# Performance work log

Measured on AMD Instinct MI355X. Metric: run time of the kernel, lower is better.

Reference implementation:

```python
import jax, jax.numpy as jnp
import numpy as np

BOS_IDX = 1
B, T, E, H, V = 32, 128, 512, 1024, 32000


def setup_inputs() -> dict:
    key = jax.random.key(0)
    ks = jax.random.split(key, 8)
    s = 0.02  # small init scale to keep gates in active range
    return {
        "encoder_outputs": jax.random.normal(ks[0], (B, T, H), jnp.float32),
        "encoder_hidden": jax.random.normal(ks[1], (1, B, H), jnp.float32),
        "target_tensor": jax.random.randint(ks[2], (B, T), 0, V),
        "embedding": jax.random.normal(ks[3], (V, E), jnp.float32) * s,
        "W_ih": jax.random.normal(ks[4], (3 * H, E), jnp.float32) * s,
        "W_hh": jax.random.normal(ks[5], (3 * H, H), jnp.float32) * s,
        "b_ih": jnp.zeros((3 * H,), jnp.float32),
        "b_hh": jnp.zeros((3 * H,), jnp.float32),
        "W_out": jax.random.normal(ks[6], (V, H), jnp.float32) * s,
        "b_out": jnp.zeros((V,), jnp.float32),
    }


def _gru_cell(x, h, W_ih, W_hh, b_ih, b_hh):
    # PyTorch GRUCell math, gate order (r, z, n)
    gi = x @ W_ih.T + b_ih          # [B, 3H]
    gh = h @ W_hh.T + b_hh          # [B, 3H]
    i_r, i_z, i_n = jnp.split(gi, 3, axis=-1)
    h_r, h_z, h_n = jnp.split(gh, 3, axis=-1)
    r = jax.nn.sigmoid(i_r + h_r)
    z = jax.nn.sigmoid(i_z + h_z)
    n = jnp.tanh(i_n + r * h_n)
    return (1.0 - z) * n + z * h


def reference(encoder_outputs, encoder_hidden, target_tensor, embedding,
              W_ih, W_hh, b_ih, b_hh, W_out, b_out):
    Bv, Tv = target_tensor.shape
    # teacher forcing: inputs are [BOS, target[:, 0], ..., target[:, T-2]]
    bos = jnp.full((Bv, 1), BOS_IDX, dtype=target_tensor.dtype)
    tokens = jnp.concatenate([bos, target_tensor[:, :-1]], axis=1)  # [B, T]
    h0 = encoder_hidden[0]  # num_layers == 1 -> [B, H]

    def step(h, tok):
        x = jax.nn.relu(embedding[tok])                    # [B, E]
        h_new = _gru_cell(x, h, W_ih, W_hh, b_ih, b_hh)    # [B, H]
        logits = h_new @ W_out.T + b_out                   # [B, V]
        return h_new, logits

    h_final, logits = jax.lax.scan(step, h0, tokens.T)     # logits: [T, B, V]
    log_probs = jax.nn.log_softmax(jnp.transpose(logits, (1, 0, 2)), axis=-1)
    return log_probs, h_final[None]  # decoder_hidden = [1, B, H]
```

## Files before the change

kernel.cpp:

```cpp
#include <hip/hip_runtime.h>

using u16 = unsigned short;
using u32 = unsigned int;
using u64 = unsigned long long;
typedef __attribute__((ext_vector_type(8))) short bf16x8;
typedef __attribute__((ext_vector_type(4))) float f32x4;

#define B_ 32
#define T_ 128
#define E_ 512
#define H_ 1024
#define V_ 32000
#define NROW 4096
#define BTV ((size_t)B_ * T_ * V_)
#define NREC 32
#define NWK 224
#define GRID_MEGA (NREC + NWK)
#define NTN 250
#define NTILES (32 * NTN)
#define NT_STRIDE 256

#define AGENT __HIP_MEMORY_SCOPE_AGENT
#define RLX __ATOMIC_RELAXED

__device__ __forceinline__ u16 f2bf(float f) {
  u32 x = __float_as_uint(f);
  x += 0x7FFFu + ((x >> 16) & 1u);
  return (u16)(x >> 16);
}

__device__ __forceinline__ void gload_lds16(const void* g, void* l) {
  __builtin_amdgcn_global_load_lds(
      (const __attribute__((address_space(1))) u32*)g,
      (__attribute__((address_space(3))) u32*)l, 16, 0, 0);
}

__device__ __forceinline__ float sigm(float x) { return 1.f / (1.f + __expf(-x)); }

__global__ void cast_bf16_kernel(const float* __restrict__ src, u16* __restrict__ dst, int n4) {
  int i = blockIdx.x * blockDim.x + threadIdx.x;
  int stride = gridDim.x * blockDim.x;
  for (; i < n4; i += stride) {
    float4 v = reinterpret_cast<const float4*>(src)[i];
    u32 p0 = (u32)f2bf(v.x) | ((u32)f2bf(v.y) << 16);
    u32 p1 = (u32)f2bf(v.z) | ((u32)f2bf(v.w) << 16);
    reinterpret_cast<uint2*>(dst)[i] = make_uint2(p0, p1);
  }
}

__global__ void embed_kernel(const int* __restrict__ tgt, const float* __restrict__ emb,
                             u16* __restrict__ X) {
  int r = blockIdx.x * 2 + (threadIdx.x >> 7);
  int c = threadIdx.x & 127;
  int t = r & 127;
  int tok = (t == 0) ? 1 : tgt[r - 1];
  float4 v = reinterpret_cast<const float4*>(emb + (size_t)tok * E_)[c];
  u32 p0 = (u32)f2bf(fmaxf(v.x, 0.f)) | ((u32)f2bf(fmaxf(v.y, 0.f)) << 16);
  u32 p1 = (u32)f2bf(fmaxf(v.z, 0.f)) | ((u32)f2bf(fmaxf(v.w, 0.f)) << 16);
  reinterpret_cast<uint2*>(X + (size_t)r * E_)[c] = make_uint2(p0, p1);
}

__global__ __launch_bounds__(256)
void gemm_bt_kernel(const u16* __restrict__ A, const u16* __restrict__ B,
                    const float* __restrict__ bias, float* __restrict__ C,
                    int K, int N) {
  __shared__ __align__(16) u16 As[128 * 32];
  __shared__ __align__(16) u16 Bs[128 * 32];
  int bid = blockIdx.x;
  int mtile = bid & 31, ntile = bid >> 5;
  int m0 = mtile << 7, n0 = ntile << 7;
  int tid = threadIdx.x, wv = tid >> 6, ln = tid & 63;
  int lr = ln & 15, lg = ln >> 4;
  int wrow = (wv >> 1) << 6, wcol = (wv & 1) << 6;

  f32x4 acc[4][4];
#pragma unroll
  for (int m = 0; m < 4; ++m)
#pragma unroll
    for (int n = 0; n < 4; ++n) acc[m][n] = (f32x4){0.f, 0.f, 0.f, 0.f};

  int c0 = tid, c1 = tid + 256;
  const u16* gA0 = A + (size_t)(m0 + (c0 >> 2)) * K + ((c0 & 3) << 3);
  const u16* gA1 = A + (size_t)(m0 + (c1 >> 2)) * K + ((c1 & 3) << 3);
  const u16* gB0 = B + (size_t)(n0 + (c0 >> 2)) * K + ((c0 & 3) << 3);
  const u16* gB1 = B + (size_t)(n0 + (c1 >> 2)) * K + ((c1 & 3) << 3);
  u16* lA0 = As + (wv << 9);
  u16* lA1 = As + 2048 + (wv << 9);
  u16* lB0 = Bs + (wv << 9);
  u16* lB1 = Bs + 2048 + (wv << 9);

  for (int k0 = 0; k0 < K; k0 += 32) {
    gload_lds16(gA0 + k0, lA0);
    gload_lds16(gA1 + k0, lA1);
    gload_lds16(gB0 + k0, lB0);
    gload_lds16(gB1 + k0, lB1);
    __syncthreads();
    bf16x8 a[4], b[4];
#pragma unroll
    for (int m = 0; m < 4; ++m)
      a[m] = *reinterpret_cast<const bf16x8*>(&As[(wrow + (m << 4) + lr) * 32 + (lg << 3)]);
#pragma unroll
    for (int n = 0; n < 4; ++n)
      b[n] = *reinterpret_cast<const bf16x8*>(&Bs[(wcol + (n << 4) + lr) * 32 + (lg << 3)]);
#pragma unroll
    for (int m = 0; m < 4; ++m)
#pragma unroll
      for (int n = 0; n < 4; ++n)
        acc[m][n] = __builtin_amdgcn_mfma_f32_16x16x32_bf16(a[m], b[n], acc[m][n], 0, 0, 0);
    __syncthreads();
  }

#pragma unroll
  for (int m = 0; m < 4; ++m) {
    int rowb = m0 + wrow + (m << 4) + (lg << 2);
#pragma unroll
    for (int n = 0; n < 4; ++n) {
      int col = n0 + wcol + (n << 4) + lr;
      float bvn = bias[col];
#pragma unroll
      for (int i = 0; i < 4; ++i)
        C[(size_t)(rowb + i) * N + col] = acc[m][n][i] + bvn;
    }
  }
}

__global__ __launch_bounds__(256)
void mega_kernel(const u16* __restrict__ Whh16, const float* __restrict__ Gi,
                 const float* __restrict__ bhh, const float* __restrict__ enc_h,
                 u16* __restrict__ hb16, u16* __restrict__ Hall,
                 const u16* __restrict__ Wout16,
                 const float* __restrict__ bout, float* __restrict__ out,
                 float* __restrict__ pM, float* __restrict__ pS,
                 float* __restrict__ outTail, u32* __restrict__ flags) {
  __shared__ __align__(16) char smem[49152];
  int bid = blockIdx.x, tid = threadIdx.x;
  int wv = tid >> 6, ln = tid & 63, lr = ln & 15, lg = ln >> 4;

  if (bid < NREC) {
    int j0 = bid << 5;
    int kb = wv << 8;
    float (*red)[2][6][256] = (float(*)[2][6][256])smem;

    bf16x8 wf[6][8];
#pragma unroll
    for (int g = 0; g < 3; ++g)
#pragma unroll
      for (int nh = 0; nh < 2; ++nh) {
        const u16* wrow = Whh16 + (size_t)(g * H_ + j0 + nh * 16 + lr) * H_ + kb + (lg << 3);
#pragma unroll
        for (int kk = 0; kk < 8; ++kk)
          wf[g * 2 + nh][kk] = *reinterpret_cast<const bf16x8*>(wrow + kk * 32);
      }

    int bb = tid >> 3;
    int j4 = (tid & 7) << 2;
    float4 bhr = *reinterpret_cast<const float4*>(bhh + 0 * H_ + j0 + j4);
    float4 bhz = *reinterpret_cast<const float4*>(bhh + 1 * H_ + j0 + j4);
    float4 bhn = *reinterpret_cast<const float4*>(bhh + 2 * H_ + j0 + j4);
    float4 hp = *reinterpret_cast<const float4*>(enc_h + bb * H_ + j0 + j4);

    for (int t = 0; t < T_; ++t) {
      int cur = t & 1, nxt = cur ^ 1;

      const float* gib = Gi + (size_t)(bb * T_ + t) * (3 * H_) + j0 + j4;
      float4 gir = *reinterpret_cast<const float4*>(gib + 0 * H_);
      float4 giz = *reinterpret_cast<const float4*>(gib + 1 * H_);
      float4 gin = *reinterpret_cast<const float4*>(gib + 2 * H_);

      if (t > 0) {
        if (ln < 8) {
          while (__hip_atomic_load(&flags[(wv * 8 + ln) * 16], RLX, AGENT) < (u32)t)
            __builtin_amdgcn_s_sleep(1);
        }
      }

      const u16* hbase = hb16 + (size_t)cur * (B_ * H_) + kb + (lg << 3);
      f32x4 acc[2][6];
#pragma unroll
      for (int mt = 0; mt < 2; ++mt)
#pragma unroll
        for (int tn = 0; tn < 6; ++tn) acc[mt][tn] = (f32x4){0.f, 0.f, 0.f, 0.f};
#pragma unroll
      for (int kk = 0; kk < 8; ++kk) {
        const u64* p0 = reinterpret_cast<const u64*>(hbase + (size_t)lr * H_ + kk * 32);
        const u64* p1 = reinterpret_cast<const u64*>(hbase + (size_t)(16 + lr) * H_ + kk * 32);
        union { u64 q[2]; bf16x8 v; } A0, A1;
        A0.q[0] = __hip_atomic_load(p0, RLX, AGENT);
        A0.q[1] = __hip_atomic_load(p0 + 1, RLX, AGENT);
        A1.q[0] = __hip_atomic_load(p1, RLX, AGENT);
        A1.q[1] = __hip_atomic_load(p1 + 1, RLX, AGENT);
#pragma unroll
        for (int tn = 0; tn < 6; ++tn) {
          acc[0][tn] = __builtin_amdgcn_mfma_f32_16x16x32_bf16(A0.v, wf[tn][kk], acc[0][tn], 0, 0, 0);
          acc[1][tn] = __builtin_amdgcn_mfma_f32_16x16x32_bf16(A1.v, wf[tn][kk], acc[1][tn], 0, 0, 0);
        }
      }

#pragma unroll
      for (int mt = 0; mt < 2; ++mt)
#pragma unroll
        for (int tn = 0; tn < 6; ++tn)
#pragma unroll
          for (int i = 0; i < 4; ++i)
            red[wv][mt][tn][((lg << 2) + i) * 16 + lr] = acc[mt][tn][i];
      __syncthreads();

      int mt = bb >> 4;
      int nh = j4 >> 4;
      int rbase = (bb & 15) * 16 + (j4 & 15);
      float4 s[3];
#pragma unroll
      for (int g = 0; g < 3; ++g) {
        float4 a4 = make_float4(0.f, 0.f, 0.f, 0.f);
#pragma unroll
        for (int w = 0; w < 4; ++w) {
          float4 v = *reinterpret_cast<const float4*>(&red[w][mt][g * 2 + nh][rbase]);
          a4.x += v.x; a4.y += v.y; a4.z += v.z; a4.w += v.w;
        }
        s[g] = a4;
      }

      float hn[4];
      {
        float r0 = sigm(gir.x + s[0].x + bhr.x);
        float r1 = sigm(gir.y + s[0].y + bhr.y);
        float r2 = sigm(gir.z + s[0].z + bhr.z);
        float r3 = sigm(gir.w + s[0].w + bhr.w);
        float z0 = sigm(giz.x + s[1].x + bhz.x);
        float z1 = sigm(giz.y + s[1].y + bhz.y);
        float z2 = sigm(giz.z + s[1].z + bhz.z);
        float z3 = sigm(giz.w + s[1].w + bhz.w);
        float a0 = gin.x + r0 * (s[2].x + bhn.x);
        float a1 = gin.y + r1 * (s[2].y + bhn.y);
        float a2 = gin.z + r2 * (s[2].z + bhn.z);
        float a3 = gin.w + r3 * (s[2].w + bhn.w);
        float n0 = 2.f / (1.f + __expf(-2.f * a0)) - 1.f;
        float n1 = 2.f / (1.f + __expf(-2.f * a1)) - 1.f;
        float n2 = 2.f / (1.f + __expf(-2.f * a2)) - 1.f;
        float n3 = 2.f / (1.f + __expf(-2.f * a3)) - 1.f;
        hn[0] = (1.f - z0) * n0 + z0 * hp.x;
        hn[1] = (1.f - z1) * n1 + z1 * hp.y;
        hn[2] = (1.f - z2) * n2 + z2 * hp.z;
        hn[3] = (1.f - z3) * n3 + z3 * hp.w;
        hp = make_float4(hn[0], hn[1], hn[2], hn[3]);
      }

      u32 p0 = (u32)f2bf(hn[0]) | ((u32)f2bf(hn[1]) << 16);
      u32 p1 = (u32)f2bf(hn[2]) | ((u32)f2bf(hn[3]) << 16);
      u64 pv = (u64)p0 | ((u64)p1 << 32);

      __hip_atomic_store(reinterpret_cast<u64*>(Hall + (size_t)(t * B_ + bb) * H_ + j0 + j4),
                         pv, RLX, AGENT);
      if (t < T_ - 1) {
        __hip_atomic_store(reinterpret_cast<u64*>(hb16 + (size_t)nxt * (B_ * H_) + bb * H_ + j0 + j4),
                           pv, RLX, AGENT);
      } else {
        reinterpret_cast<float4*>(outTail + (size_t)bb * H_ + j0 + j4)[0] = hp;
      }
      __syncthreads();
      if (tid == 0)
        __hip_atomic_store(&flags[bid * 16], (u32)(t + 1), RLX, AGENT);
    }
    return;
  }

  int wid = bid - NREC;
  u16* As = (u16*)smem;
  u16* Bs = (u16*)(smem + 8192);
  float* pmh = (float*)(smem + 16384);
  float* psh = (float*)(smem + 17408);
  int wrow = (wv >> 1) << 6, wcol = (wv & 1) << 6;

  for (int tau = wid; tau < NTILES; tau += NWK) {
    int m = tau / NTN, n = tau - m * NTN;
    int target = 4 * (m + 1);
    if (tid < NREC) {
      while ((int)__hip_atomic_load(&flags[tid * 16], RLX, AGENT) < target)
        __builtin_amdgcn_s_sleep(32);
    }
    __syncthreads();

    int m0 = m << 7, n0 = n << 7;
    f32x4 acc[4][4];
#pragma unroll
    for (int mi = 0; mi < 4; ++mi)
#pragma unroll
      for (int ni = 0; ni < 4; ++ni) acc[mi][ni] = (f32x4){0.f, 0.f, 0.f, 0.f};

    int c0 = tid, c1 = tid + 256;
    const u16* gA0 = Hall + (size_t)(m0 + (c0 >> 2)) * H_ + ((c0 & 3) << 3);
    const u16* gA1 = Hall + (size_t)(m0 + (c1 >> 2)) * H_ + ((c1 & 3) << 3);
    const u16* gB0 = Wout16 + (size_t)(n0 + (c0 >> 2)) * H_ + ((c0 & 3) << 3);
    const u16* gB1 = Wout16 + (size_t)(n0 + (c1 >> 2)) * H_ + ((c1 & 3) << 3);
    u16* lA0 = As + (wv << 9);
    u16* lA1 = As + 2048 + (wv << 9);
    u16* lB0 = Bs + (wv << 9);
    u16* lB1 = Bs + 2048 + (wv << 9);

    for (int k0 = 0; k0 < H_; k0 += 32) {
      gload_lds16(gA0 + k0, lA0);
      gload_lds16(gA1 + k0, lA1);
      gload_lds16(gB0 + k0, lB0);
      gload_lds16(gB1 + k0, lB1);
      __syncthreads();
      bf16x8 a[4], b[4];
#pragma unroll
      for (int mi = 0; mi < 4; ++mi)
        a[mi] = *reinterpret_cast<const bf16x8*>(&As[(wrow + (mi << 4) + lr) * 32 + (lg << 3)]);
#pragma unroll
      for (int ni = 0; ni < 4; ++ni)
        b[ni] = *reinterpret_cast<const bf16x8*>(&Bs[(wcol + (ni << 4) + lr) * 32 + (lg << 3)]);
#pragma unroll
      for (int mi = 0; mi < 4; ++mi)
#pragma unroll
        for (int ni = 0; ni < 4; ++ni)
          acc[mi][ni] = __builtin_amdgcn_mfma_f32_16x16x32_bf16(a[mi], b[ni], acc[mi][ni], 0, 0, 0);
      __syncthreads();
    }

    float bv[4];
#pragma unroll
    for (int ni = 0; ni < 4; ++ni) bv[ni] = bout[n0 + wcol + (ni << 4) + lr];

#pragma unroll
    for (int mi = 0; mi < 4; ++mi) {
#pragma unroll
      for (int i = 0; i < 4; ++i) {
        int row = wrow + (mi << 4) + (lg << 2) + i;
        int r = m0 + row;
        int rg = (r & 31) * T_ + (r >> 5);
        float* crow = out + (size_t)rg * V_;
        float v[4];
#pragma unroll
        for (int ni = 0; ni < 4; ++ni) {
          v[ni] = acc[mi][ni][i] + bv[ni];
          crow[n0 + wcol + (ni << 4) + lr] = v[ni];
        }
        float vm = fmaxf(fmaxf(v[0], v[1]), fmaxf(v[2], v[3]));
        vm = fmaxf(vm, __shfl_xor(vm, 1));
        vm = fmaxf(vm, __shfl_xor(vm, 2));
        vm = fmaxf(vm, __shfl_xor(vm, 4));
        vm = fmaxf(vm, __shfl_xor(vm, 8));
        float se = __expf(v[0] - vm) + __expf(v[1] - vm) +
                   __expf(v[2] - vm) + __expf(v[3] - vm);
        se += __shfl_xor(se, 1);
        se += __shfl_xor(se, 2);
        se += __shfl_xor(se, 4);
        se += __shfl_xor(se, 8);
        if (lr == 0) { pmh[(wv & 1) * 128 + row] = vm; psh[(wv & 1) * 128 + row] = se; }
      }
    }
    __syncthreads();
    if (tid < 128) {
      float m0v = pmh[tid], m1v = pmh[128 + tid];
      float M = fmaxf(m0v, m1v);
      float S = psh[tid] * __expf(m0v - M) + psh[128 + tid] * __expf(m1v - M);
      int r = m0 + tid;
      int rg = (r & 31) * T_ + (r >> 5);
      pM[(size_t)rg * NT_STRIDE + n] = M;
      pS[(size_t)rg * NT_STRIDE + n] = S;
    }
    __syncthreads();
  }
}

__global__ __launch_bounds__(512)
void lse_fused_kernel(const float* __restrict__ pM, const float* __restrict__ pS,
                      float* __restrict__ out) {
  int r = blockIdx.x;
  int tid = threadIdx.x, wv = tid >> 6, ln = tid & 63;
  float M = -3.0e38f, S = 0.f;
  if (tid < NTN) { M = pM[(size_t)r * NT_STRIDE + tid]; S = pS[(size_t)r * NT_STRIDE + tid]; }
#pragma unroll
  for (int o = 32; o; o >>= 1) {
    float Mo = __shfl_xor(M, o);
    float So = __shfl_xor(S, o);
    float Mn = fmaxf(M, Mo);
    S = S * __expf(M - Mn) + So * __expf(Mo - Mn);
    M = Mn;
  }
  __shared__ float tM[8], tS[8], lsh;
  if (ln == 0) { tM[wv] = M; tS[wv] = S; }
  __syncthreads();
  if (tid == 0) {
    float Mf = tM[0], Sf = tS[0];
    for (int w = 1; w < 8; ++w) {
      float Mn = fmaxf(Mf, tM[w]);
      Sf = Sf * __expf(Mf - Mn) + tS[w] * __expf(tM[w] - Mn);
      Mf = Mn;
    }
    lsh = Mf + __logf(Sf);
  }
  __syncthreads();
  float l = lsh;
  float4* p = reinterpret_cast<float4*>(out + (size_t)r * V_);
  for (int i = tid; i < V_ / 4; i += 512) {
    float4 v = p[i];
    v.x -= l; v.y -= l; v.z -= l; v.w -= l;
    p[i] = v;
  }
}

extern "C" void kernel_launch(void* const* d_in, const int* in_sizes, int n_in,
                              void* d_out, int out_size, void* d_ws, size_t ws_size,
                              hipStream_t stream) {
  const float* enc_h = (const float*)d_in[1];
  const int*   tgt   = (const int*)d_in[2];
  const float* emb   = (const float*)d_in[3];
  const float* Wih   = (const float*)d_in[4];
  const float* Whh   = (const float*)d_in[5];
  const float* bih   = (const float*)d_in[6];
  const float* bhh   = (const float*)d_in[7];
  const float* Wout  = (const float*)d_in[8];
  const float* bout  = (const float*)d_in[9];
  float* out = (float*)d_out;

  char* ws = (char*)d_ws;
  size_t off = 0;
  auto alloc = [&](size_t bytes) -> void* {
    void* p = ws + off;
    off = (off + bytes + 255) & ~(size_t)255;
    return p;
  };
  u32*  flags  = (u32*)alloc(4096);
  u16*  Wih16  = (u16*)alloc((size_t)3 * H_ * E_ * 2);
  u16*  Whh16  = (u16*)alloc((size_t)3 * H_ * H_ * 2);
  u16*  Wout16 = (u16*)alloc((size_t)V_ * H_ * 2);
  u16*  X16    = (u16*)alloc((size_t)NROW * E_ * 2);
  u16*  Hall   = (u16*)alloc((size_t)NROW * H_ * 2);
  u16*  hb16   = (u16*)alloc((size_t)2 * B_ * H_ * 2);
  float* Gi    = (float*)alloc((size_t)NROW * 3 * H_ * 4);
  float* pM    = (float*)alloc((size_t)NROW * NT_STRIDE * 4);
  float* pS    = (float*)alloc((size_t)NROW * NT_STRIDE * 4);

  hipMemsetAsync(flags, 0, 4096, stream);
  cast_bf16_kernel<<<1024, 256, 0, stream>>>(Wih, Wih16, 3 * H_ * E_ / 4);
  cast_bf16_kernel<<<1024, 256, 0, stream>>>(Whh, Whh16, 3 * H_ * H_ / 4);
  cast_bf16_kernel<<<2048, 256, 0, stream>>>(Wout, Wout16, V_ * H_ / 4);
  cast_bf16_kernel<<<32, 256, 0, stream>>>(enc_h, hb16, B_ * H_ / 4);
  embed_kernel<<<NROW / 2, 256, 0, stream>>>(tgt, emb, X16);

  gemm_bt_kernel<<<(3 * H_ / 128) * 32, 256, 0, stream>>>(X16, Wih16, bih, Gi, E_, 3 * H_);

  mega_kernel<<<GRID_MEGA, 256, 0, stream>>>(Whh16, Gi, bhh, enc_h, hb16, Hall,
                                             Wout16, bout, out, pM, pS,
                                             out + BTV, flags);

  lse_fused_kernel<<<NROW, 512, 0, stream>>>(pM, pS, out);
}
```

Baseline: 1.226 ms.

## Fuse log-softmax normalization into mega kernel with per-chunk completion counters

Removes the separate LSE kernel and instead has worker blocks, two m-chunks behind, wait on a per-chunk done counter and then normalize the completed rows inside the persistent kernel. The goal is to overlap the log-softmax pass over the output with the recurrent and output GEMM work rather than running it afterward. Output and partial stores become relaxed agent-scope atomics so other blocks can see them, and the tile loop is restructured per m. This adds spin-waits and extra synchronization to the worker blocks and could stall GEMM progress. It also relies on relaxed atomics for cross-block visibility without explicit fences.

```diff
diff --git a/kernel.cpp b/kernel.cpp
--- a/kernel.cpp
+++ b/kernel.cpp
@@ -17,7 +17,6 @@
 #define NWK 224
 #define GRID_MEGA (NREC + NWK)
 #define NTN 250
-#define NTILES (32 * NTN)
 #define NT_STRIDE 256
 
 #define AGENT __HIP_MEMORY_SCOPE_AGENT
@@ -131,7 +130,8 @@
                  const u16* __restrict__ Wout16,
                  const float* __restrict__ bout, float* __restrict__ out,
                  float* __restrict__ pM, float* __restrict__ pS,
-                 float* __restrict__ outTail, u32* __restrict__ flags) {
+                 float* __restrict__ outTail, u32* __restrict__ flags,
+                 u32* __restrict__ done) {
   __shared__ __align__(16) char smem[49152];
   int bid = blockIdx.x, tid = threadIdx.x;
   int wv = tid >> 6, ln = tid & 63, lr = ln & 15, lg = ln >> 4;
@@ -269,135 +269,151 @@
   u16* Bs = (u16*)(smem + 8192);
   float* pmh = (float*)(smem + 16384);
   float* psh = (float*)(smem + 17408);
+  float* sred = (float*)smem;
   int wrow = (wv >> 1) << 6, wcol = (wv & 1) << 6;
 
-  for (int tau = wid; tau < NTILES; tau += NWK) {
-    int m = tau / NTN, n = tau - m * NTN;
-    int target = 4 * (m + 1);
-    if (tid < NREC) {
-      while ((int)__hip_atomic_load(&flags[tid * 16], RLX, AGENT) < target)
-        __builtin_amdgcn_s_sleep(32);
+  for (int m = 0; m < 33; ++m) {
+    if (m < 32) {
+      int target = 4 * (m + 1);
+      if (tid < NREC) {
+        while ((int)__hip_atomic_load(&flags[tid * 16], RLX, AGENT) < target)
+          __builtin_amdgcn_s_sleep(64);
+      }
+      __syncthreads();
+
+      for (int n = wid; n < NTN; n += NWK) {
+        int m0 = m << 7, n0 = n << 7;
+        f32x4 acc[4][4];
+#pragma unroll
+        for (int mi = 0; mi < 4; ++mi)
+#pragma unroll
+          for (int ni = 0; ni < 4; ++ni) acc[mi][ni] = (f32x4){0.f, 0.f, 0.f, 0.f};
+
+        int c0 = tid, c1 = tid + 256;
+        const u16* gA0 = Hall + (size_t)(m0 + (c0 >> 2)) * H_ + ((c0 & 3) << 3);
+        const u16* gA1 = Hall + (size_t)(m0 + (c1 >> 2)) * H_ + ((c1 & 3) << 3);
+        const u16* gB0 = Wout16 + (size_t)(n0 + (c0 >> 2)) * H_ + ((c0 & 3) << 3);
+        const u16* gB1 = Wout16 + (size_t)(n0 + (c1 >> 2)) * H_ + ((c1 & 3) << 3);
+        u16* lA0 = As + (wv << 9);
+        u16* lA1 = As + 2048 + (wv << 9);
+        u16* lB0 = Bs + (wv << 9);
+        u16* lB1 = Bs + 2048 + (wv << 9);
+
+        for (int k0 = 0; k0 < H_; k0 += 32) {
+          gload_lds16(gA0 + k0, lA0);
+          gload_lds16(gA1 + k0, lA1);
+          gload_lds16(gB0 + k0, lB0);
+          gload_lds16(gB1 + k0, lB1);
+          __syncthreads();
+          bf16x8 a[4], b[4];
+#pragma unroll
+          for (int mi = 0; mi < 4; ++mi)
+            a[mi] = *reinterpret_cast<const bf16x8*>(&As[(wrow + (mi << 4) + lr) * 32 + (lg << 3)]);
+#pragma unroll
+          for (int ni = 0; ni < 4; ++ni)
+            b[ni] = *reinterpret_cast<const bf16x8*>(&Bs[(wcol + (ni << 4) + lr) * 32 + (lg << 3)]);
+#pragma unroll
+          for (int mi = 0; mi < 4; ++mi)
+#pragma unroll
+            for (int ni = 0; ni < 4; ++ni)
+              acc[mi][ni] = __builtin_amdgcn_mfma_f32_16x16x32_bf16(a[mi], b[ni], acc[mi][ni], 0, 0, 0);
+          __syncthreads();
+        }
+
+        float bv[4];
+#pragma unroll
+        for (int ni = 0; ni < 4; ++ni) bv[ni] = bout[n0 + wcol + (ni << 4) + lr];
+
+#pragma unroll
+        for (int mi = 0; mi < 4; ++mi) {
+#pragma unroll
+          for (int i = 0; i < 4; ++i) {
+            int row = wrow + (mi << 4) + (lg << 2) + i;
+            int r = m0 + row;
+            int rg = (r & 31) * T_ + (r >> 5);
+            float* crow = out + (size_t)rg * V_;
+            float v[4];
+#pragma unroll
+            for (int ni = 0; ni < 4; ++ni) {
+              v[ni] = acc[mi][ni][i] + bv[ni];
+              __hip_atomic_store(crow + n0 + wcol + (ni << 4) + lr, v[ni], RLX, AGENT);
+            }
+            float vm = fmaxf(fmaxf(v[0], v[1]), fmaxf(v[2], v[3]));
+            vm = fmaxf(vm, __shfl_xor(vm, 1));
+            vm = fmaxf(vm, __shfl_xor(vm, 2));
+            vm = fmaxf(vm, __shfl_xor(vm, 4));
+            vm = fmaxf(vm, __shfl_xor(vm, 8));
+            float se = __expf(v[0] - vm) + __expf(v[1] - vm) +
+                       __expf(v[2] - vm) + __expf(v[3] - vm);
+            se += __shfl_xor(se, 1);
+            se += __shfl_xor(se, 2);
+            se += __shfl_xor(se, 4);
+            se += __shfl_xor(se, 8);
+            if (lr == 0) { pmh[(wv & 1) * 128 + row] = vm; psh[(wv & 1) * 128 + row] = se; }
+          }
+        }
+        __syncthreads();
+        if (tid < 128) {
+          float m0v = pmh[tid], m1v = pmh[128 + tid];
+          float M = fmaxf(m0v, m1v);
+          float S = psh[tid] * __expf(m0v - M) + psh[128 + tid] * __expf(m1v - M);
+          int r = m0 + tid;
+          int rg = (r & 31) * T_ + (r >> 5);
+          __hip_atomic_store(&pM[(size_t)rg * NT_STRIDE + n], M, RLX, AGENT);
+          __hip_atomic_store(&pS[(size_t)rg * NT_STRIDE + n], S, RLX, AGENT);
+        }
+        __syncthreads();
+        if (tid == 0) __hip_atomic_fetch_add(&done[m * 16], 1u, RLX, AGENT);
+      }
     }
-    __syncthreads();
-
-    int m0 = m << 7, n0 = n << 7;
-    f32x4 acc[4][4];
-#pragma unroll
-    for (int mi = 0; mi < 4; ++mi)
-#pragma unroll
-      for (int ni = 0; ni < 4; ++ni) acc[mi][ni] = (f32x4){0.f, 0.f, 0.f, 0.f};
-
-    int c0 = tid, c1 = tid + 256;
-    const u16* gA0 = Hall + (size_t)(m0 + (c0 >> 2)) * H_ + ((c0 & 3) << 3);
-    const u16* gA1 = Hall + (size_t)(m0 + (c1 >> 2)) * H_ + ((c1 & 3) << 3);
-    const u16* gB0 = Wout16 + (size_t)(n0 + (c0 >> 2)) * H_ + ((c0 & 3) << 3);
-    const u16* gB1 = Wout16 + (size_t)(n0 + (c1 >> 2)) * H_ + ((c1 & 3) << 3);
-    u16* lA0 = As + (wv << 9);
-    u16* lA1 = As + 2048 + (wv << 9);
-    u16* lB0 = Bs + (wv << 9);
-    u16* lB1 = Bs + 2048 + (wv << 9);
-
-    for (int k0 = 0; k0 < H_; k0 += 32) {
-      gload_lds16(gA0 + k0, lA0);
-      gload_lds16(gA1 + k0, lA1);
-      gload_lds16(gB0 + k0, lB0);
-      gload_lds16(gB1 + k0, lB1);
-      __syncthreads();
-      bf16x8 a[4], b[4];
-#pragma unroll
-      for (int mi = 0; mi < 4; ++mi)
-        a[mi] = *reinterpret_cast<const bf16x8*>(&As[(wrow + (mi << 4) + lr) * 32 + (lg << 3)]);
-#pragma unroll
-      for (int ni = 0; ni < 4; ++ni)
-        b[ni] = *reinterpret_cast<const bf16x8*>(&Bs[(wcol + (ni << 4) + lr) * 32 + (lg << 3)]);
-#pragma unroll
-      for (int mi = 0; mi < 4; ++mi)
-#pragma unroll
-        for (int ni = 0; ni < 4; ++ni)
-          acc[mi][ni] = __builtin_amdgcn_mfma_f32_16x16x32_bf16(a[mi], b[ni], acc[mi][ni], 0, 0, 0);
-      __syncthreads();
+
+    int pcLo = (m == 32) ? 30 : m - 2;
+    int pcHi = (m == 32) ? 31 : m - 2;
+    for (int pc = pcLo; pc <= pcHi; ++pc) {
+      if (pc < 0) continue;
+      if (wid < 128) {
+        if (tid == 0) {
+          while (__hip_atomic_load(&done[pc * 16], RLX, AGENT) < (u32)NTN)
+            __builtin_amdgcn_s_sleep(16);
+        }
+        __syncthreads();
+        int r = pc * 128 + wid;
+        int rg = (r & 31) * T_ + (r >> 5);
+        float M = -3.0e38f, S = 0.f;
+        if (tid < NTN) {
+          M = pM[(size_t)rg * NT_STRIDE + tid];
+          S = pS[(size_t)rg * NT_STRIDE + tid];
+        }
+#pragma unroll
+        for (int o = 32; o; o >>= 1) {
+          float Mo = __shfl_xor(M, o);
+          float So = __shfl_xor(S, o);
+          float Mn = fmaxf(M, Mo);
+          S = S * __expf(M - Mn) + So * __expf(Mo - Mn);
+          M = Mn;
+        }
+        if (ln == 0) { sred[wv] = M; sred[8 + wv] = S; }
+        __syncthreads();
+        if (tid == 0) {
+          float Mf = sred[0], Sf = sred[8];
+          for (int w = 1; w < 4; ++w) {
+            float Mn = fmaxf(Mf, sred[w]);
+            Sf = Sf * __expf(Mf - Mn) + sred[8 + w] * __expf(sred[w] - Mn);
+            Mf = Mn;
+          }
+          sred[12] = Mf + __logf(Sf);
+        }
+        __syncthreads();
+        float l = sred[12];
+        float4* p = reinterpret_cast<float4*>(out + (size_t)rg * V_);
+        for (int i = tid; i < V_ / 4; i += 256) {
+          float4 v = p[i];
+          v.x -= l; v.y -= l; v.z -= l; v.w -= l;
+          p[i] = v;
+        }
+        __syncthreads();
+      }
     }
-
-    float bv[4];
-#pragma unroll
-    for (int ni = 0; ni < 4; ++ni) bv[ni] = bout[n0 + wcol + (ni << 4) + lr];
-
-#pragma unroll
-    for (int mi = 0; mi < 4; ++mi) {
-#pragma unroll
-      for (int i = 0; i < 4; ++i) {
-        int row = wrow + (mi << 4) + (lg << 2) + i;
-        int r = m0 + row;
-        int rg = (r & 31) * T_ + (r >> 5);
-        float* crow = out + (size_t)rg * V_;
-        float v[4];
-#pragma unroll
-        for (int ni = 0; ni < 4; ++ni) {
-          v[ni] = acc[mi][ni][i] + bv[ni];
-          crow[n0 + wcol + (ni << 4) + lr] = v[ni];
-        }
-        float vm = fmaxf(fmaxf(v[0], v[1]), fmaxf(v[2], v[3]));
-        vm = fmaxf(vm, __shfl_xor(vm, 1));
-        vm = fmaxf(vm, __shfl_xor(vm, 2));
-        vm = fmaxf(vm, __shfl_xor(vm, 4));
-        vm = fmaxf(vm, __shfl_xor(vm, 8));
-        float se = __expf(v[0] - vm) + __expf(v[1] - vm) +
-                   __expf(v[2] - vm) + __expf(v[3] - vm);
-        se += __shfl_xor(se, 1);
-        se += __shfl_xor(se, 2);
-        se += __shfl_xor(se, 4);
-        se += __shfl_xor(se, 8);
-        if (lr == 0) { pmh[(wv & 1) * 128 + row] = vm; psh[(wv & 1) * 128 + row] = se; }
-      }
-    }
-    __syncthreads();
-    if (tid < 128) {
-      float m0v = pmh[tid], m1v = pmh[128 + tid];
-      float M = fmaxf(m0v, m1v);
-      float S = psh[tid] * __expf(m0v - M) + psh[128 + tid] * __expf(m1v - M);
-      int r = m0 + tid;
-      int rg = (r & 31) * T_ + (r >> 5);
-      pM[(size_t)rg * NT_STRIDE + n] = M;
-      pS[(size_t)rg * NT_STRIDE + n] = S;
-    }
-    __syncthreads();
-  }
-}
-
-__global__ __launch_bounds__(512)
-void lse_fused_kernel(const float* __restrict__ pM, const float* __restrict__ pS,
-                      float* __restrict__ out) {
-  int r = blockIdx.x;
-  int tid = threadIdx.x, wv = tid >> 6, ln = tid & 63;
-  float M = -3.0e38f, S = 0.f;
-  if (tid < NTN) { M = pM[(size_t)r * NT_STRIDE + tid]; S = pS[(size_t)r * NT_STRIDE + tid]; }
-#pragma unroll
-  for (int o = 32; o; o >>= 1) {
-    float Mo = __shfl_xor(M, o);
-    float So = __shfl_xor(S, o);
-    float Mn = fmaxf(M, Mo);
-    S = S * __expf(M - Mn) + So * __expf(Mo - Mn);
-    M = Mn;
-  }
-  __shared__ float tM[8], tS[8], lsh;
-  if (ln == 0) { tM[wv] = M; tS[wv] = S; }
-  __syncthreads();
-  if (tid == 0) {
-    float Mf = tM[0], Sf = tS[0];
-    for (int w = 1; w < 8; ++w) {
-      float Mn = fmaxf(Mf, tM[w]);
-      Sf = Sf * __expf(Mf - Mn) + tS[w] * __expf(tM[w] - Mn);
-      Mf = Mn;
-    }
-    lsh = Mf + __logf(Sf);
-  }
-  __syncthreads();
-  float l = lsh;
-  float4* p = reinterpret_cast<float4*>(out + (size_t)r * V_);
-  for (int i = tid; i < V_ / 4; i += 512) {
-    float4 v = p[i];
-    v.x -= l; v.y -= l; v.z -= l; v.w -= l;
-    p[i] = v;
   }
 }
 
@@ -423,6 +439,7 @@
     return p;
   };
   u32*  flags  = (u32*)alloc(4096);
+  u32*  done   = (u32*)alloc(4096);
   u16*  Wih16  = (u16*)alloc((size_t)3 * H_ * E_ * 2);
   u16*  Whh16  = (u16*)alloc((size_t)3 * H_ * H_ * 2);
   u16*  Wout16 = (u16*)alloc((size_t)V_ * H_ * 2);
@@ -433,7 +450,7 @@
   float* pM    = (float*)alloc((size_t)NROW * NT_STRIDE * 4);
   float* pS    = (float*)alloc((size_t)NROW * NT_STRIDE * 4);
 
-  hipMemsetAsync(flags, 0, 4096, stream);
+  hipMemsetAsync(flags, 0, 8192, stream);
   cast_bf16_kernel<<<1024, 256, 0, stream>>>(Wih, Wih16, 3 * H_ * E_ / 4);
   cast_bf16_kernel<<<1024, 256, 0, stream>>>(Whh, Whh16, 3 * H_ * H_ / 4);
   cast_bf16_kernel<<<2048, 256, 0, stream>>>(Wout, Wout16, V_ * H_ / 4);
@@ -444,7 +461,5 @@
 
   mega_kernel<<<GRID_MEGA, 256, 0, stream>>>(Whh16, Gi, bhh, enc_h, hb16, Hall,
                                              Wout16, bout, out, pM, pS,
-                                             out + BTV, flags);
-
-  lse_fused_kernel<<<NROW, 512, 0, stream>>>(pM, pS, out);
-}
+                                             out + BTV, flags, done);
+}
```

After: 1.944 ms. +58.5%, slower.

## Overlap Wout bf16 cast with recurrence and add aggregated progress flag

Applied to the files above, without the earlier changes.

Moves the Wout fp32-to-bf16 cast out of its own kernel and into the worker blocks of the persistent mega kernel, so it runs while the recurrent blocks start the GRU. Each worker now owns a fixed set of vocabulary columns across all 32 time chunks. That means it converts only its own Wout rows and needs no cross-block synchronisation for them. One block is given over to an aggregator wave that reduces the 32 recurrence flags into a single counter, so workers poll one word instead of 32. The cost is one fewer GEMM worker (223 instead of 224) and possible load imbalance, since 250 column tiles spread over 223 workers leaves some workers with two tiles.

```diff
diff --git a/kernel.cpp b/kernel.cpp
--- a/kernel.cpp
+++ b/kernel.cpp
@@ -14,10 +14,9 @@
 #define NROW 4096
 #define BTV ((size_t)B_ * T_ * V_)
 #define NREC 32
-#define NWK 224
-#define GRID_MEGA (NREC + NWK)
+#define NWKG 223
+#define GRID_MEGA 256
 #define NTN 250
-#define NTILES (32 * NTN)
 #define NT_STRIDE 256
 
 #define AGENT __HIP_MEMORY_SCOPE_AGENT
@@ -128,10 +127,11 @@
 void mega_kernel(const u16* __restrict__ Whh16, const float* __restrict__ Gi,
                  const float* __restrict__ bhh, const float* __restrict__ enc_h,
                  u16* __restrict__ hb16, u16* __restrict__ Hall,
-                 const u16* __restrict__ Wout16,
+                 const float* __restrict__ Wout, u16* __restrict__ Wout16,
                  const float* __restrict__ bout, float* __restrict__ out,
                  float* __restrict__ pM, float* __restrict__ pS,
-                 float* __restrict__ outTail, u32* __restrict__ flags) {
+                 float* __restrict__ outTail, u32* __restrict__ flags,
+                 u32* __restrict__ agg) {
   __shared__ __align__(16) char smem[49152];
   int bid = blockIdx.x, tid = threadIdx.x;
   int wv = tid >> 6, ln = tid & 63, lr = ln & 15, lg = ln >> 4;
@@ -265,102 +265,136 @@
   }
 
   int wid = bid - NREC;
+
+  if (wid == NWKG) {
+    if (wv == 0) {
+      u32 pub = 0;
+      while (pub < (u32)T_) {
+        u32 v = __hip_atomic_load(&flags[(ln & 31) * 16], RLX, AGENT);
+#pragma unroll
+        for (int o = 16; o; o >>= 1) {
+          u32 vo = (u32)__shfl_xor((int)v, o);
+          v = v < vo ? v : vo;
+        }
+        if (v > pub) {
+          pub = v;
+          if (ln == 0) __hip_atomic_store(&agg[0], pub, RLX, AGENT);
+        } else {
+          __builtin_amdgcn_s_sleep(2);
+        }
+      }
+    }
+    return;
+  }
+
   u16* As = (u16*)smem;
   u16* Bs = (u16*)(smem + 8192);
   float* pmh = (float*)(smem + 16384);
   float* psh = (float*)(smem + 17408);
   int wrow = (wv >> 1) << 6, wcol = (wv & 1) << 6;
 
-  for (int tau = wid; tau < NTILES; tau += NWK) {
-    int m = tau / NTN, n = tau - m * NTN;
+  for (int n = wid; n < NTN; n += NWKG) {
+    const float4* src = reinterpret_cast<const float4*>(Wout + (size_t)n * 128 * H_);
+    uint2* dst = reinterpret_cast<uint2*>(Wout16 + (size_t)n * 128 * H_);
+    for (int i = tid; i < 128 * H_ / 4; i += 256) {
+      float4 v = src[i];
+      dst[i] = make_uint2((u32)f2bf(v.x) | ((u32)f2bf(v.y) << 16),
+                          (u32)f2bf(v.z) | ((u32)f2bf(v.w) << 16));
+    }
+  }
+  __syncthreads();
+
+  for (int m = 0; m < 32; ++m) {
     int target = 4 * (m + 1);
-    if (tid < NREC) {
-      while ((int)__hip_atomic_load(&flags[tid * 16], RLX, AGENT) < target)
-        __builtin_amdgcn_s_sleep(32);
+    if (tid == 0) {
+      while ((int)__hip_atomic_load(&agg[0], RLX, AGENT) < target)
+        __builtin_amdgcn_s_sleep(64);
     }
     __syncthreads();
 
-    int m0 = m << 7, n0 = n << 7;
-    f32x4 acc[4][4];
-#pragma unroll
-    for (int mi = 0; mi < 4; ++mi)
-#pragma unroll
-      for (int ni = 0; ni < 4; ++ni) acc[mi][ni] = (f32x4){0.f, 0.f, 0.f, 0.f};
-
-    int c0 = tid, c1 = tid + 256;
-    const u16* gA0 = Hall + (size_t)(m0 + (c0 >> 2)) * H_ + ((c0 & 3) << 3);
-    const u16* gA1 = Hall + (size_t)(m0 + (c1 >> 2)) * H_ + ((c1 & 3) << 3);
-    const u16* gB0 = Wout16 + (size_t)(n0 + (c0 >> 2)) * H_ + ((c0 & 3) << 3);
-    const u16* gB1 = Wout16 + (size_t)(n0 + (c1 >> 2)) * H_ + ((c1 & 3) << 3);
-    u16* lA0 = As + (wv << 9);
-    u16* lA1 = As + 2048 + (wv << 9);
-    u16* lB0 = Bs + (wv << 9);
-    u16* lB1 = Bs + 2048 + (wv << 9);
-
-    for (int k0 = 0; k0 < H_; k0 += 32) {
-      gload_lds16(gA0 + k0, lA0);
-      gload_lds16(gA1 + k0, lA1);
-      gload_lds16(gB0 + k0, lB0);
-      gload_lds16(gB1 + k0, lB1);
+    for (int n = wid; n < NTN; n += NWKG) {
+      int m0 = m << 7, n0 = n << 7;
+      f32x4 acc[4][4];
+#pragma unroll
+      for (int mi = 0; mi < 4; ++mi)
+#pragma unroll
+        for (int ni = 0; ni < 4; ++ni) acc[mi][ni] = (f32x4){0.f, 0.f, 0.f, 0.f};
+
+      int c0 = tid, c1 = tid + 256;
+      const u16* gA0 = Hall + (size_t)(m0 + (c0 >> 2)) * H_ + ((c0 & 3) << 3);
+      const u16* gA1 = Hall + (size_t)(m0 + (c1 >> 2)) * H_ + ((c1 & 3) << 3);
+      const u16* gB0 = Wout16 + (size_t)(n0 + (c0 >> 2)) * H_ + ((c0 & 3) << 3);
+      const u16* gB1 = Wout16 + (size_t)(n0 + (c1 >> 2)) * H_ + ((c1 & 3) << 3);
+      u16* lA0 = As + (wv << 9);
+      u16* lA1 = As + 2048 + (wv << 9);
+      u16* lB0 = Bs + (wv << 9);
+      u16* lB1 = Bs + 2048 + (wv << 9);
+
+      for (int k0 = 0; k0 < H_; k0 += 32) {
+        gload_lds16(gA0 + k0, lA0);
+        gload_lds16(gA1 + k0, lA1);
+        gload_lds16(gB0 + k0, lB0);
+        gload_lds16(gB1 + k0, lB1);
+        __syncthreads();
+        bf16x8 a[4], b[4];
+#pragma unroll
+        for (int mi = 0; mi < 4; ++mi)
+          a[mi] = *reinterpret_cast<const bf16x8*>(&As[(wrow + (mi << 4) + lr) * 32 + (lg << 3)]);
+#pragma unroll
+        for (int ni = 0; ni < 4; ++ni)
+          b[ni] = *reinterpret_cast<const bf16x8*>(&Bs[(wcol + (ni << 4) + lr) * 32 + (lg << 3)]);
+#pragma unroll
+        for (int mi = 0; mi < 4; ++mi)
+#pragma unroll
+          for (int ni = 0; ni < 4; ++ni)
+            acc[mi][ni] = __builtin_amdgcn_mfma_f32_16x16x32_bf16(a[mi], b[ni], acc[mi][ni], 0, 0, 0);
+        __syncthreads();
+      }
+
+      float bv[4];
+#pragma unroll
+      for (int ni = 0; ni < 4; ++ni) bv[ni] = bout[n0 + wcol + (ni << 4) + lr];
+
+#pragma unroll
+      for (int mi = 0; mi < 4; ++mi) {
+#pragma unroll
+        for (int i = 0; i < 4; ++i) {
+          int row = wrow + (mi << 4) + (lg << 2) + i;
+          int r = m0 + row;
+          int rg = (r & 31) * T_ + (r >> 5);
+          float* crow = out + (size_t)rg * V_;
+          float v[4];
+#pragma unroll
+          for (int ni = 0; ni < 4; ++ni) {
+            v[ni] = acc[mi][ni][i] + bv[ni];
+            crow[n0 + wcol + (ni << 4) + lr] = v[ni];
+          }
+          float vm = fmaxf(fmaxf(v[0], v[1]), fmaxf(v[2], v[3]));
+          vm = fmaxf(vm, __shfl_xor(vm, 1));
+          vm = fmaxf(vm, __shfl_xor(vm, 2));
+          vm = fmaxf(vm, __shfl_xor(vm, 4));
+          vm = fmaxf(vm, __shfl_xor(vm, 8));
+          float se = __expf(v[0] - vm) + __expf(v[1] - vm) +
+                     __expf(v[2] - vm) + __expf(v[3] - vm);
+          se += __shfl_xor(se, 1);
+          se += __shfl_xor(se, 2);
+          se += __shfl_xor(se, 4);
+          se += __shfl_xor(se, 8);
+          if (lr == 0) { pmh[(wv & 1) * 128 + row] = vm; psh[(wv & 1) * 128 + row] = se; }
+        }
+      }
       __syncthreads();
-      bf16x8 a[4], b[4];
-#pragma unroll
-      for (int mi = 0; mi < 4; ++mi)
-        a[mi] = *reinterpret_cast<const bf16x8*>(&As[(wrow + (mi << 4) + lr) * 32 + (lg << 3)]);
-#pragma unroll
-      for (int ni = 0; ni < 4; ++ni)
-        b[ni] = *reinterpret_cast<const bf16x8*>(&Bs[(wcol + (ni << 4) + lr) * 32 + (lg << 3)]);
-#pragma unroll
-      for (int mi = 0; mi < 4; ++mi)
-#pragma unroll
-        for (int ni = 0; ni < 4; ++ni)
-          acc[mi][ni] = __builtin_amdgcn_mfma_f32_16x16x32_bf16(a[mi], b[ni], acc[mi][ni], 0, 0, 0);
+      if (tid < 128) {
+        float m0v = pmh[tid], m1v = pmh[128 + tid];
+        float M = fmaxf(m0v, m1v);
+        float S = psh[tid] * __expf(m0v - M) + psh[128 + tid] * __expf(m1v - M);
+        int r = m0 + tid;
+        int rg = (r & 31) * T_ + (r >> 5);
+        pM[(size_t)rg * NT_STRIDE + n] = M;
+        pS[(size_t)rg * NT_STRIDE + n] = S;
+      }
       __syncthreads();
     }
-
-    float bv[4];
-#pragma unroll
-    for (int ni = 0; ni < 4; ++ni) bv[ni] = bout[n0 + wcol + (ni << 4) + lr];
-
-#pragma unroll
-    for (int mi = 0; mi < 4; ++mi) {
-#pragma unroll
-      for (int i = 0; i < 4; ++i) {
-        int row = wrow + (mi << 4) + (lg << 2) + i;
-        int r = m0 + row;
-        int rg = (r & 31) * T_ + (r >> 5);
-        float* crow = out + (size_t)rg * V_;
-        float v[4];
-#pragma unroll
-        for (int ni = 0; ni < 4; ++ni) {
-          v[ni] = acc[mi][ni][i] + bv[ni];
-          crow[n0 + wcol + (ni << 4) + lr] = v[ni];
-        }
-        float vm = fmaxf(fmaxf(v[0], v[1]), fmaxf(v[2], v[3]));
-        vm = fmaxf(vm, __shfl_xor(vm, 1));
-        vm = fmaxf(vm, __shfl_xor(vm, 2));
-        vm = fmaxf(vm, __shfl_xor(vm, 4));
-        vm = fmaxf(vm, __shfl_xor(vm, 8));
-        float se = __expf(v[0] - vm) + __expf(v[1] - vm) +
-                   __expf(v[2] - vm) + __expf(v[3] - vm);
-        se += __shfl_xor(se, 1);
-        se += __shfl_xor(se, 2);
-        se += __shfl_xor(se, 4);
-        se += __shfl_xor(se, 8);
-        if (lr == 0) { pmh[(wv & 1) * 128 + row] = vm; psh[(wv & 1) * 128 + row] = se; }
-      }
-    }
-    __syncthreads();
-    if (tid < 128) {
-      float m0v = pmh[tid], m1v = pmh[128 + tid];
-      float M = fmaxf(m0v, m1v);
-      float S = psh[tid] * __expf(m0v - M) + psh[128 + tid] * __expf(m1v - M);
-      int r = m0 + tid;
-      int rg = (r & 31) * T_ + (r >> 5);
-      pM[(size_t)rg * NT_STRIDE + n] = M;
-      pS[(size_t)rg * NT_STRIDE + n] = S;
-    }
-    __syncthreads();
   }
 }
 
@@ -423,6 +457,7 @@
     return p;
   };
   u32*  flags  = (u32*)alloc(4096);
+  u32*  agg    = (u32*)alloc(4096);
   u16*  Wih16  = (u16*)alloc((size_t)3 * H_ * E_ * 2);
   u16*  Whh16  = (u16*)alloc((size_t)3 * H_ * H_ * 2);
   u16*  Wout16 = (u16*)alloc((size_t)V_ * H_ * 2);
@@ -433,18 +468,17 @@
   float* pM    = (float*)alloc((size_t)NROW * NT_STRIDE * 4);
   float* pS    = (float*)alloc((size_t)NROW * NT_STRIDE * 4);
 
-  hipMemsetAsync(flags, 0, 4096, stream);
+  hipMemsetAsync(flags, 0, 8192, stream);
   cast_bf16_kernel<<<1024, 256, 0, stream>>>(Wih, Wih16, 3 * H_ * E_ / 4);
   cast_bf16_kernel<<<1024, 256, 0, stream>>>(Whh, Whh16, 3 * H_ * H_ / 4);
-  cast_bf16_kernel<<<2048, 256, 0, stream>>>(Wout, Wout16, V_ * H_ / 4);
   cast_bf16_kernel<<<32, 256, 0, stream>>>(enc_h, hb16, B_ * H_ / 4);
   embed_kernel<<<NROW / 2, 256, 0, stream>>>(tgt, emb, X16);
 
   gemm_bt_kernel<<<(3 * H_ / 128) * 32, 256, 0, stream>>>(X16, Wih16, bih, Gi, E_, 3 * H_);
 
   mega_kernel<<<GRID_MEGA, 256, 0, stream>>>(Whh16, Gi, bhh, enc_h, hb16, Hall,
-                                             Wout16, bout, out, pM, pS,
-                                             out + BTV, flags);
+                                             Wout, Wout16, bout, out, pM, pS,
+                                             out + BTV, flags, agg);
 
   lse_fused_kernel<<<NROW, 512, 0, stream>>>(pM, pS, out);
 }
```

After: 1.782 ms. 1.45x slower.
